# Performance work log

Measured on AMD Instinct MI355X. Metric: run time of the kernel, lower is better.

Reference implementation:

```python
import jax, jax.numpy as jnp
import numpy as np

T_STEPS, N = 8192, 2048
SPIKE_THRESHOLD = 30.0


def setup_inputs() -> dict:
    key = jax.random.key(0)
    k_x, k_w = jax.random.split(key, 2)
    w_mean, w_var = 0.15, 0.25
    x_in = jax.random.normal(k_x, (T_STEPS, N), dtype=jnp.float32)
    # rand_ws = w_mean - w_var + 2*w_var*rand(N,N)
    w = w_mean - w_var + 2.0 * w_var * jax.random.uniform(k_w, (N, N), dtype=jnp.float32)
    v_rest = jnp.full((N,), -65.0, dtype=jnp.float32)
    tau_m = jnp.full((N,), 4.0, dtype=jnp.float32)
    tau_g = jnp.full((N,), 2.0, dtype=jnp.float32)
    pre_c = jnp.float32(4.0)
    post_c = jnp.float32(130.0)
    v0 = jnp.zeros((N,), dtype=jnp.float32)
    g0 = jnp.zeros((N,), dtype=jnp.float32)
    return {"x_in": x_in, "w": w, "v_rest": v_rest, "tau_m": tau_m,
            "tau_g": tau_g, "pre_c": pre_c, "post_c": post_c, "v0": v0, "g0": g0}


def reference(x_in, w, v_rest, tau_m, tau_g, pre_c, post_c, v0, g0):
    # Faithful LIF_complex.forward, iterated over T timesteps via lax.scan.
    def step(carry, x_t):
        v, g = carry
        # synaptic input current
        I = post_c * jax.nn.sigmoid(pre_c * (w @ g + x_t))
        # conductance decay
        g = g - g / tau_g
        # membrane potential update
        v = v + (v_rest - v + I) / tau_m
        # soft spike surrogate (returned), hard spike for reset
        spiked_soft = jax.nn.sigmoid(v - SPIKE_THRESHOLD)
        spk = (v >= SPIKE_THRESHOLD).astype(v.dtype)
        not_spk = 1.0 - spk
        v = spk * v_rest + not_spk * v
        g = spk + not_spk * g
        return (v, g), (v, spiked_soft)

    _, (vs, spikeds) = jax.lax.scan(step, (v0, g0), x_in)
    # [2, T, N]: vs and soft-spike traces over time
    return jnp.stack([vs, spikeds])
```

## Files before the change

### kernel.cpp

```cpp
#include <hip/hip_runtime.h>
#include <cmath>


#define T_STEPS 8192
#define NN      2048
#define NBLK    128
#define NTHR    1024
#define RPB     16
#define DUMP    64
#define NSLOT   128
#define PADU    16

typedef unsigned long long u64;

__device__ __forceinline__ float stable_sigmoid(float x) {
    if (x >= 0.0f) {
        return 1.0f / (1.0f + expf(-x));
    } else {
        float e = expf(x);
        return e / (1.0f + e);
    }
}

#define DPP_ADD(acc, ctrl, rmask)                                         \
    acc += __int_as_float(__builtin_amdgcn_update_dpp(                    \
        0, __float_as_int(acc), ctrl, rmask, 0xF, true));

#define WAVE_RED(acc)            \
    DPP_ADD(acc, 0x111, 0xF)     \
    DPP_ADD(acc, 0x112, 0xF)     \
    DPP_ADD(acc, 0x114, 0xF)     \
    DPP_ADD(acc, 0x118, 0xF)     \
    DPP_ADD(acc, 0x142, 0xA)     \
    DPP_ADD(acc, 0x143, 0xC)

__global__ __launch_bounds__(NTHR, 2) void lif_kernel(
    const float* __restrict__ x_in,
    const float* __restrict__ w,
    const float* __restrict__ v_rest,
    const float* __restrict__ tau_m,
    const float* __restrict__ tau_g,
    const float* __restrict__ pre_cp,
    const float* __restrict__ post_cp,
    const float* __restrict__ v0,
    const float* __restrict__ g0,
    float* __restrict__ out,
    u64* __restrict__ slots)
{
    __shared__ unsigned sbits[NSLOT];
    __shared__ float preduce[2][4][RPB];
    __shared__ float vbuf[2][DUMP][RPB];
    __shared__ float sbuf[2][DUMP][RPB];

    const int tid = threadIdx.x;
    const int b   = blockIdx.x;
    const int wv  = tid >> 6;
    const int i   = wv & 3;
    const int j   = wv >> 2;
    const int k   = tid & 63;

    const float* wbase = w + (size_t)(b * RPB + 4 * i) * NN + 512 * j;
    const float4* r0 = (const float4*)(wbase);
    const float4* r1 = (const float4*)(wbase + NN);
    const float4* r2 = (const float4*)(wbase + 2 * NN);
    const float4* r3 = (const float4*)(wbase + 3 * NN);
    const float4 w0a = r0[2 * k], w0b = r0[2 * k + 1];
    const float4 w1a = r1[2 * k], w1b = r1[2 * k + 1];
    const float4 w2a = r2[2 * k], w2b = r2[2 * k + 1];
    const float4 w3a = r3[2 * k], w3b = r3[2 * k + 1];

    const int c0 = 512 * j + 8 * k;
    float4 ga = ((const float4*)(g0 + c0))[0];
    float4 gb = ((const float4*)(g0 + c0))[1];
    const float4 tga = ((const float4*)(tau_g + c0))[0];
    const float4 tgb = ((const float4*)(tau_g + c0))[1];
    const float4 rga = make_float4(1.0f / tga.x, 1.0f / tga.y,
                                   1.0f / tga.z, 1.0f / tga.w);
    const float4 rgb = make_float4(1.0f / tgb.x, 1.0f / tgb.y,
                                   1.0f / tgb.z, 1.0f / tgb.w);
    const int slot_i  = c0 >> 4;
    const int bitbase = c0 & 15;

    const float pre_c  = pre_cp[0];
    const float post_c = post_cp[0];

    float vr = 0.f, rtm = 0.f, v = 0.f;
    if (tid < RPB) {
        const int n = b * RPB + tid;
        vr  = v_rest[n];
        rtm = 1.0f / tau_m[n];
        v   = v0[n];
    }

    for (int t = 0; t < T_STEPS; ++t) {
        float x = 0.0f;
        if (tid < RPB) x = x_in[(size_t)t * NN + b * RPB + tid];

        float4 da = ga, db = gb;
        if (t != 0) {
            da.x = fmaf(-rga.x, ga.x, ga.x); da.y = fmaf(-rga.y, ga.y, ga.y);
            da.z = fmaf(-rga.z, ga.z, ga.z); da.w = fmaf(-rga.w, ga.w, ga.w);
            db.x = fmaf(-rgb.x, gb.x, gb.x); db.y = fmaf(-rgb.y, gb.y, gb.y);
            db.z = fmaf(-rgb.z, gb.z, gb.z); db.w = fmaf(-rgb.w, gb.w, gb.w);

            if (wv < 2) {
                const int s = (wv << 6) | k;
                const u64* sl = slots +
                    ((size_t)((t - 1) & 1) * NSLOT + s) * PADU;
                const unsigned want = (unsigned)(t - 1);
                u64 A = __hip_atomic_load(sl, __ATOMIC_RELAXED,
                                          __HIP_MEMORY_SCOPE_AGENT);
                while ((unsigned)(A >> 32) != want) {
                    __builtin_amdgcn_s_sleep(1);
                    A = __hip_atomic_load(sl, __ATOMIC_RELAXED,
                                          __HIP_MEMORY_SCOPE_AGENT);
                }
                sbits[s] = (unsigned)A;
            }
        }
        __syncthreads();

        if (t != 0) {
            const unsigned bits = sbits[slot_i] >> bitbase;
            ga.x = (bits &   1u) ? 1.0f : da.x;
            ga.y = (bits &   2u) ? 1.0f : da.y;
            ga.z = (bits &   4u) ? 1.0f : da.z;
            ga.w = (bits &   8u) ? 1.0f : da.w;
            gb.x = (bits &  16u) ? 1.0f : db.x;
            gb.y = (bits &  32u) ? 1.0f : db.y;
            gb.z = (bits &  64u) ? 1.0f : db.z;
            gb.w = (bits & 128u) ? 1.0f : db.w;
        }

        float a0 = 0.f, a1 = 0.f, a2 = 0.f, a3 = 0.f;
#define ROWFMA(acc, wa, wb)                                       \
        acc = fmaf(wa.x, ga.x, acc); acc = fmaf(wa.y, ga.y, acc); \
        acc = fmaf(wa.z, ga.z, acc); acc = fmaf(wa.w, ga.w, acc); \
        acc = fmaf(wb.x, gb.x, acc); acc = fmaf(wb.y, gb.y, acc); \
        acc = fmaf(wb.z, gb.z, acc); acc = fmaf(wb.w, gb.w, acc);
        ROWFMA(a0, w0a, w0b)
        ROWFMA(a1, w1a, w1b)
        ROWFMA(a2, w2a, w2b)
        ROWFMA(a3, w3a, w3b)
#undef ROWFMA
        WAVE_RED(a0)
        WAVE_RED(a1)
        WAVE_RED(a2)
        WAVE_RED(a3)
        if (k == 63)
            ((float4*)preduce[t & 1])[j * 4 + i] = make_float4(a0, a1, a2, a3);
        __syncthreads();

        if (tid < RPB) {
            const float* pr = (const float*)preduce[t & 1];
            float u = (pr[tid] + pr[tid + 16]) + (pr[tid + 32] + pr[tid + 48]);
            float I = post_c * stable_sigmoid(pre_c * (u + x));
            v = v + (vr - v + I) * rtm;
            bool spk = (v >= 30.0f);
            u64 bal = __ballot(spk);
            if (tid == 0) {
                u64 pk = ((u64)(unsigned)t << 32) | (bal & 0xFFFFull);
                __hip_atomic_store(slots + ((size_t)(t & 1) * NSLOT + b) * PADU,
                                   pk, __ATOMIC_RELAXED,
                                   __HIP_MEMORY_SCOPE_AGENT);
            }
            __builtin_amdgcn_sched_barrier(0);
            float soft = stable_sigmoid(v - 30.0f);
            v = spk ? vr : v;
            vbuf[(t >> 6) & 1][t & (DUMP - 1)][tid] = v;
            sbuf[(t >> 6) & 1][t & (DUMP - 1)][tid] = soft;
        }

        if ((t & (DUMP - 1)) == 0 && t != 0) {
            const int bb = ((t >> 6) & 1) ^ 1;
            const int t0 = t - DUMP;
            const int s  = tid >> 4;
            const int rr = tid & 15;
            size_t o = (size_t)(t0 + s) * NN + b * RPB + rr;
            out[o] = vbuf[bb][s][rr];
            out[(size_t)T_STEPS * NN + o] = sbuf[bb][s][rr];
        }
    }

    __syncthreads();
    {
        const int bb = ((T_STEPS - DUMP) >> 6) & 1;
        const int t0 = T_STEPS - DUMP;
        const int s  = tid >> 4;
        const int rr = tid & 15;
        size_t o = (size_t)(t0 + s) * NN + b * RPB + rr;
        out[o] = vbuf[bb][s][rr];
        out[(size_t)T_STEPS * NN + o] = sbuf[bb][s][rr];
    }
}

extern "C" void kernel_launch(void* const* d_in, const int* in_sizes, int n_in,
                              void* d_out, int out_size, void* d_ws, size_t ws_size,
                              hipStream_t stream) {
    const float* x_in   = (const float*)d_in[0];
    const float* w      = (const float*)d_in[1];
    const float* v_rest = (const float*)d_in[2];
    const float* tau_m  = (const float*)d_in[3];
    const float* tau_g  = (const float*)d_in[4];
    const float* pre_c  = (const float*)d_in[5];
    const float* post_c = (const float*)d_in[6];
    const float* v0     = (const float*)d_in[7];
    const float* g0     = (const float*)d_in[8];
    float* out = (float*)d_out;

    u64* slots = (u64*)d_ws;

    hipMemsetAsync(slots, 0xFF, 2 * NSLOT * PADU * sizeof(u64), stream);

    void* args[] = {
        (void*)&x_in, (void*)&w, (void*)&v_rest, (void*)&tau_m, (void*)&tau_g,
        (void*)&pre_c, (void*)&post_c, (void*)&v0, (void*)&g0,
        (void*)&out, (void*)&slots
    };
    hipLaunchCooperativeKernel((void*)lif_kernel, dim3(NBLK), dim3(NTHR),
                               args, 0, stream);
}
```

Before: 14.82 ms.

## Replace per-step block barrier with per-wave tagged LDS flag polling

Each wave now polls the global spike slots for its own row group (8 lanes per wave) and publishes them into LDS tagged with the timestep. The first __syncthreads of each step is dropped, so each wave waits only for the slots it needs via an LDS spin on the tag instead of a full block barrier. This is meant to cut barrier latency on the critical serial path. The cost is more global polling traffic and LDS spin loops, and tags are 16-bit, so timestep wraparound must still stay consistent.

```diff
diff --git a/kernel.cpp b/kernel.cpp
--- a/kernel.cpp
+++ b/kernel.cpp
@@ -81,8 +81,12 @@
     const int slot_i  = c0 >> 4;
     const int bitbase = c0 & 15;
 
+    const int rs = 32 * j + 8 * i + (k & 7);
+
     const float pre_c  = pre_cp[0];
     const float post_c = post_cp[0];
+
+    if (tid < NSLOT) sbits[tid] = 0xFFFF0000u;
 
     float vr = 0.f, rtm = 0.f, v = 0.f;
     if (tid < RPB) {
@@ -103,25 +107,38 @@
             db.x = fmaf(-rgb.x, gb.x, gb.x); db.y = fmaf(-rgb.y, gb.y, gb.y);
             db.z = fmaf(-rgb.z, gb.z, gb.z); db.w = fmaf(-rgb.w, gb.w, gb.w);
 
-            if (wv < 2) {
-                const int s = (wv << 6) | k;
+            const unsigned want = (unsigned)(t - 1);
+
+            {
                 const u64* sl = slots +
-                    ((size_t)((t - 1) & 1) * NSLOT + s) * PADU;
-                const unsigned want = (unsigned)(t - 1);
-                u64 A = __hip_atomic_load(sl, __ATOMIC_RELAXED,
-                                          __HIP_MEMORY_SCOPE_AGENT);
-                while ((unsigned)(A >> 32) != want) {
-                    __builtin_amdgcn_s_sleep(1);
-                    A = __hip_atomic_load(sl, __ATOMIC_RELAXED,
-                                          __HIP_MEMORY_SCOPE_AGENT);
+                    ((size_t)((t - 1) & 1) * NSLOT + rs) * PADU;
+                bool pending = (k < 8);
+                while (__any(pending)) {
+                    if (pending) {
+                        u64 A = __hip_atomic_load(sl, __ATOMIC_RELAXED,
+                                                  __HIP_MEMORY_SCOPE_AGENT);
+                        if ((unsigned)(A >> 32) == want) {
+                            __hip_atomic_store(
+                                &sbits[rs],
+                                (want << 16) | ((unsigned)A & 0xFFFFu),
+                                __ATOMIC_RELAXED,
+                                __HIP_MEMORY_SCOPE_WORKGROUP);
+                            pending = false;
+                        }
+                    }
+                    if (__any(pending)) __builtin_amdgcn_s_sleep(1);
                 }
-                sbits[s] = (unsigned)A;
             }
-        }
-        __syncthreads();
-
-        if (t != 0) {
-            const unsigned bits = sbits[slot_i] >> bitbase;
+
+            unsigned wval;
+            const unsigned wtag = want << 16;
+            for (;;) {
+                wval = __hip_atomic_load(&sbits[slot_i], __ATOMIC_RELAXED,
+                                         __HIP_MEMORY_SCOPE_WORKGROUP);
+                if ((wval & 0xFFFF0000u) == wtag) break;
+                __builtin_amdgcn_s_sleep(1);
+            }
+            const unsigned bits = (wval & 0xFFFFu) >> bitbase;
             ga.x = (bits &   1u) ? 1.0f : da.x;
             ga.y = (bits &   2u) ? 1.0f : da.y;
             ga.z = (bits &   4u) ? 1.0f : da.z;
```

Result: slower. 16.01 ms (+8.0%).
